# Performance work log

Measured on AMD Instinct MI355X. Metric: run time of the kernel, lower is better.

## Reference

```python
import jax, jax.numpy as jnp
import numpy as np

FRAME_LEN = 128
FFT_LEN = 128            # smallest power of 2 >= frame_length (TF default)
NUM_SPEC_BINS = FFT_LEN // 2 + 1  # 65
NUM_MEL = 80
SAMPLE_RATE = 16000.0
LOWER_HZ, UPPER_HZ = 80.0, 7600.0


def _hz_to_mel(f):
    # TF's HTK-style mel: 1127 * ln(1 + f/700)
    return 1127.0 * np.log1p(np.asarray(f, dtype=np.float64) / 700.0)


def _linear_to_mel_weight_matrix():
    # Faithful port of tf.signal.linear_to_mel_weight_matrix
    linear_freqs = np.linspace(0.0, SAMPLE_RATE / 2.0, NUM_SPEC_BINS)
    spec_mel = _hz_to_mel(linear_freqs[1:])[:, None]            # [64, 1] (bin 0 zeroed)
    edges = np.linspace(_hz_to_mel(LOWER_HZ), _hz_to_mel(UPPER_HZ), NUM_MEL + 2)
    lower, center, upper = edges[None, :-2], edges[None, 1:-1], edges[None, 2:]
    lower_slopes = (spec_mel - lower) / (center - lower)
    upper_slopes = (upper - spec_mel) / (upper - center)
    w = np.maximum(0.0, np.minimum(lower_slopes, upper_slopes))  # [64, 80]
    return np.pad(w, [[1, 0], [0, 0]]).astype(np.float32)        # [65, 80]


_MEL_W = jnp.asarray(_linear_to_mel_weight_matrix())


def setup_inputs() -> dict:
    key = jax.random.key(0)
    x = jax.random.normal(key, (16, 16384), dtype=jnp.float32)
    return {"x": x}


def reference(x):
    B, N = x.shape
    # pad_end=True with frame_step=1 -> N frames, pad FRAME_LEN-1 zeros at the end
    xp = jnp.pad(x, ((0, 0), (0, FRAME_LEN - 1)))
    idx = jnp.arange(N)[:, None] + jnp.arange(FRAME_LEN)[None, :]  # [N, 128]
    frames = xp[:, idx]                                            # [B, N, 128]
    n = jnp.arange(FRAME_LEN, dtype=jnp.float32)
    window = 0.5 - 0.5 * jnp.cos(2.0 * jnp.pi * n / FRAME_LEN)     # periodic Hann
    stft = jnp.fft.rfft(frames * window, n=FFT_LEN, axis=-1)       # [B, N, 65] complex
    mag = jax.lax.stop_gradient(jnp.abs(stft).astype(jnp.float32))
    mel = mag @ _MEL_W                                             # [B, N, 80]
    return jnp.concatenate([x[..., None], mel], axis=-1)           # [B, N, 81]
```

## Files before the change

### kernel.cpp

```cpp
#include <hip/hip_runtime.h>
#include <hip/hip_fp16.h>
#include <math.h>

#define B_SZ 16
#define N_SZ 16384
#define T_FR 128
#define NBIN 65
#define NMEL 80
#define ST   83
#define KN   6


constexpr float QC[33] = {
  1.0f,            0.99879545620f, 0.99518472667f, 0.98917650996f,
  0.98078528040f,  0.97003125319f, 0.95694033573f, 0.94154406518f,
  0.92387953251f,  0.90398929312f, 0.88192126435f, 0.85772861000f,
  0.83146961230f,  0.80320753148f, 0.77301045336f, 0.74095112535f,
  0.70710678119f,  0.67155895485f, 0.63439328416f, 0.59569930449f,
  0.55557023302f,  0.51410274419f, 0.47139673683f, 0.42755509343f,
  0.38268343236f,  0.33688985339f, 0.29028467725f, 0.24298017990f,
  0.19509032202f,  0.14673047446f, 0.09801714033f, 0.04906767433f,
  0.0f
};

__host__ __device__ constexpr float cosi(int k) {
  k = ((k % 128) + 128) % 128;
  return (k <= 32) ? QC[k]
       : (k <= 64) ? -QC[64 - k]
       : (k <= 96) ? -QC[k - 64]
       : QC[128 - k];
}
__host__ __device__ constexpr float sini(int k) { return cosi(k - 32); }
__host__ __device__ constexpr float hannw(int n) { return 0.5f - 0.5f * cosi(n); }
__host__ __device__ constexpr int rev6(int m) {
  return ((m & 1) << 5) | ((m & 2) << 3) | ((m & 4) << 1) |
         ((m & 8) >> 1) | ((m & 16) >> 3) | ((m & 32) >> 5);
}

constexpr double cln(double x) {
  int k = 0;
  while (x > 1.5)  { x *= 0.5; ++k; }
  while (x < 0.75) { x *= 2.0; --k; }
  const double y = (x - 1.0) / (x + 1.0);
  const double y2 = y * y;
  double t = y, s = 0.0;
  for (int i = 0; i < 40; ++i) { s += t / (double)(2 * i + 1); t *= y2; }
  return 2.0 * s + (double)k * 0.69314718055994530942;
}
constexpr double melf(double f) { return 1127.0 * cln(1.0 + f / 700.0); }

struct MelTab {
  int   kbe[NMEL];
  float w[NMEL][KN];
  constexpr MelTab() : kbe{}, w{} {
    const double mlo = melf(80.0), mhi = melf(7600.0);
    const double dm  = (mhi - mlo) / 81.0;
    for (int j = 0; j < NMEL; ++j) {
      const double lower = mlo + dm * (double)j;
      const double upper = lower + 2.0 * dm;
      int kb = 64;
      for (int k = 1; k < NBIN; ++k) {
        const double m = melf(125.0 * (double)k);
        const double a = m - lower, b2 = upper - m;
        if ((a < b2 ? a : b2) > 0.0) { kb = k; break; }
      }
      if (kb > NBIN - KN) kb = NBIN - KN;
      kbe[j] = kb;
      for (int r = 0; r < KN; ++r) {
        const int k = kb + r;
        double ww = 0.0;
        if (k >= 1 && k < NBIN) {
          const double m = melf(125.0 * (double)k);
          const double a = (m - lower) / dm, b2 = (upper - m) / dm;
          ww = a < b2 ? a : b2;
          if (ww < 0.0) ww = 0.0;
        }
        w[j][r] = (float)ww;
      }
    }
  }
};
constexpr MelTab MT{};


template <int LEN>
__device__ __forceinline__ void fft_stage(float (&zr)[64], float (&zi)[64]) {
#pragma unroll
  for (int i = 0; i < 64; i += LEN) {
#pragma unroll
    for (int j = 0; j < LEN / 2; ++j) {
      const int   q  = 128 * j / LEN;
      const float wr = cosi(q);
      const float wi = -sini(q);
      const int   a = i + j, bb = i + j + LEN / 2;
      const float br = zr[bb], bi = zi[bb];
      const float tr = wr * br - wi * bi;
      const float ti = wr * bi + wi * br;
      zr[bb] = zr[a] - tr;
      zi[bb] = zi[a] - ti;
      zr[a] += tr;
      zi[a] += ti;
    }
  }
}

__global__ __launch_bounds__(T_FR) void melspec_kernel(const float* __restrict__ x,
                                                       float* __restrict__ out) {
  __shared__ float  xs[T_FR + 128];
  __shared__ __half stage[T_FR * ST];

  const int tid = threadIdx.x;
  const int t0  = blockIdx.x * T_FR;
  const int b   = blockIdx.y;
  const float* xrow = x + (size_t)b * N_SZ;

  for (int i = tid; i < T_FR + 128; i += T_FR) {
    const int g = t0 + i;
    xs[i] = (g < N_SZ) ? xrow[g] : 0.0f;
  }
  __syncthreads();

  float zr[64], zi[64];
  {
    const float* xf = xs + tid;
#pragma unroll
    for (int m = 0; m < 64; ++m) {
      const int rm = rev6(m);
      zr[m] = xf[2 * rm]     * hannw(2 * rm);
      zi[m] = xf[2 * rm + 1] * hannw(2 * rm + 1);
    }
  }
  fft_stage<2>(zr, zi);
  fft_stage<4>(zr, zi);
  fft_stage<8>(zr, zi);
  fft_stage<16>(zr, zi);
  fft_stage<32>(zr, zi);
  fft_stage<64>(zr, zi);

  float mag[NBIN];
#pragma unroll
  for (int k = 0; k < NBIN; ++k) {
    const int ka = k & 63, kc = (64 - k) & 63;
    const float Ar = zr[ka], Ai = zi[ka];
    const float Br = zr[kc], Bi = zi[kc];
    const float c = cosi(k), s = sini(k);
    const float Xr = (Ar + Br) + c * (Ai + Bi) - s * (Ar - Br);
    const float Xi = (Ai - Bi) - c * (Ar - Br) - s * (Ai + Bi);
    mag[k] = 0.5f * sqrtf(Xr * Xr + Xi * Xi);
  }

  {
    __half* srow = stage + tid * ST;
    srow[0] = __float2half(xs[tid]);
#pragma unroll
    for (int j = 0; j < NMEL; ++j) {
      const int kb = MT.kbe[j];
      float acc = MT.w[j][0] * mag[kb];
#pragma unroll
      for (int r = 1; r < KN; ++r)
        acc = fmaf(MT.w[j][r], mag[kb + r], acc);
      srow[1 + j] = __float2half(acc);
    }
  }

  __syncthreads();

  float* orow = out + ((size_t)b * N_SZ + t0) * 81;
  int t = (tid >= 81) ? 1 : 0;
  int c = (tid >= 81) ? tid - 81 : tid;
  for (int i = 0; i < 81; ++i) {
    orow[i * T_FR + tid] = __half2float(stage[t * ST + c]);
    t += 1;
    c += 47;
    if (c >= 81) { c -= 81; ++t; }
  }
}

extern "C" void kernel_launch(void* const* d_in, const int* in_sizes, int n_in,
                              void* d_out, int out_size, void* d_ws, size_t ws_size,
                              hipStream_t stream) {
  const float* x = (const float*)d_in[0];
  float* out = (float*)d_out;
  dim3 grid(N_SZ / T_FR, B_SZ);
  dim3 block(T_FR);
  hipLaunchKernelGGL(melspec_kernel, grid, block, 0, stream, x, out);
}
```

Measured before the change: 119.0 us.

## Split each frame's FFT across two threads and partition mel projection across halves

Doubles the block to 256 threads so each 128-point FFT frame is handled by a thread pair. Each thread runs a 32-point FFT and the final radix-2 stage is done with cross-lane shuffles. Magnitudes are staged in shared memory as half precision, then the two thread halves each compute 40 mel bins using compile-time sparse filter tables. The intent is to cut per-thread register pressure (the 64-element complex arrays) and raise occupancy and parallelism. The cost is extra shuffles, an extra shared-memory pass and sync, and more fp16 rounding.

```diff
diff --git a/kernel.cpp b/kernel.cpp
--- a/kernel.cpp
+++ b/kernel.cpp
@@ -5,10 +5,12 @@
 #define B_SZ 16
 #define N_SZ 16384
 #define T_FR 128
+#define BLK  256
 #define NBIN 65
 #define NMEL 80
-#define ST   83
-#define KN   6
+#define MST  66
+#define SST  82
+#define KN2  5
 
 
 constexpr float QC[33] = {
@@ -22,7 +24,6 @@
   0.19509032202f,  0.14673047446f, 0.09801714033f, 0.04906767433f,
   0.0f
 };
-
 __host__ __device__ constexpr float cosi(int k) {
   k = ((k % 128) + 128) % 128;
   return (k <= 32) ? QC[k]
@@ -49,44 +50,49 @@
 }
 constexpr double melf(double f) { return 1127.0 * cln(1.0 + f / 700.0); }
 
-struct MelTab {
-  int   kbe[NMEL];
-  float w[NMEL][KN];
-  constexpr MelTab() : kbe{}, w{} {
+struct MelTab2 {
+  int   kb[NMEL];
+  float w[NMEL][KN2];
+  bool  ok0, ok1, okw;
+  constexpr MelTab2() : kb{}, w{}, ok0(true), ok1(true), okw(true) {
     const double mlo = melf(80.0), mhi = melf(7600.0);
     const double dm  = (mhi - mlo) / 81.0;
     for (int j = 0; j < NMEL; ++j) {
       const double lower = mlo + dm * (double)j;
       const double upper = lower + 2.0 * dm;
-      int kb = 64;
+      int b0 = -1, b1 = -1;
       for (int k = 1; k < NBIN; ++k) {
         const double m = melf(125.0 * (double)k);
-        const double a = m - lower, b2 = upper - m;
-        if ((a < b2 ? a : b2) > 0.0) { kb = k; break; }
-      }
-      if (kb > NBIN - KN) kb = NBIN - KN;
-      kbe[j] = kb;
-      for (int r = 0; r < KN; ++r) {
-        const int k = kb + r;
+        if (m - lower > 0.0 && upper - m > 0.0) { if (b0 < 0) b0 = k; b1 = k; }
+      }
+      if (b0 < 0) { b0 = 1; b1 = 0; }
+      kb[j] = b0;
+      for (int r = 0; r < KN2; ++r) {
+        const int k = b0 + r;
         double ww = 0.0;
-        if (k >= 1 && k < NBIN) {
+        if (k <= b1) {
           const double m = melf(125.0 * (double)k);
-          const double a = (m - lower) / dm, b2 = (upper - m) / dm;
-          ww = a < b2 ? a : b2;
-          if (ww < 0.0) ww = 0.0;
+          const double a = (m - lower) / dm, c = (upper - m) / dm;
+          ww = a < c ? a : c; if (ww < 0.0) ww = 0.0;
         }
         w[j][r] = (float)ww;
       }
+      if (b1 - b0 + 1 > KN2) okw = false;
+      if (j < 40) { if (b1 > 15) ok0 = false; }
+      else        { if (b0 < 12 || b1 > 64) ok1 = false; }
     }
   }
 };
-constexpr MelTab MT{};
+constexpr MelTab2 MT{};
+static_assert(MT.okw, "mel filter support wider than KN2");
+static_assert(MT.ok0, "low-half filters exceed bin 15");
+static_assert(MT.ok1, "high-half filters outside bins 12..64");
 
 
 template <int LEN>
-__device__ __forceinline__ void fft_stage(float (&zr)[64], float (&zi)[64]) {
-#pragma unroll
-  for (int i = 0; i < 64; i += LEN) {
+__device__ __forceinline__ void fft_stage32(float (&zr)[32], float (&zi)[32]) {
+#pragma unroll
+  for (int i = 0; i < 32; i += LEN) {
 #pragma unroll
     for (int j = 0; j < LEN / 2; ++j) {
       const int   q  = 128 * j / LEN;
@@ -104,75 +110,173 @@
   }
 }
 
-__global__ __launch_bounds__(T_FR) void melspec_kernel(const float* __restrict__ x,
-                                                       float* __restrict__ out) {
-  __shared__ float  xs[T_FR + 128];
-  __shared__ __half stage[T_FR * ST];
-
-  const int tid = threadIdx.x;
-  const int t0  = blockIdx.x * T_FR;
-  const int b   = blockIdx.y;
+__global__ __launch_bounds__(BLK) void melspec_kernel(const float* __restrict__ x,
+                                                      float* __restrict__ out) {
+  __shared__ float  xs[BLK];
+  __shared__ __half mags[T_FR * MST];
+  __shared__ __half stage[T_FR * SST];
+
+  const int i  = threadIdx.x;
+  const int t0 = blockIdx.x * T_FR;
+  const int b  = blockIdx.y;
   const float* xrow = x + (size_t)b * N_SZ;
 
-  for (int i = tid; i < T_FR + 128; i += T_FR) {
+  {
     const int g = t0 + i;
     xs[i] = (g < N_SZ) ? xrow[g] : 0.0f;
   }
   __syncthreads();
 
-  float zr[64], zi[64];
-  {
-    const float* xf = xs + tid;
-#pragma unroll
-    for (int m = 0; m < 64; ++m) {
+  const int t = i >> 1, h = i & 1;
+  float zr[32], zi[32];
+  {
+    const float* xf = xs + t;
+#pragma unroll
+    for (int m = 0; m < 32; ++m) {
       const int rm = rev6(m);
-      zr[m] = xf[2 * rm]     * hannw(2 * rm);
-      zi[m] = xf[2 * rm + 1] * hannw(2 * rm + 1);
-    }
-  }
-  fft_stage<2>(zr, zi);
-  fft_stage<4>(zr, zi);
-  fft_stage<8>(zr, zi);
-  fft_stage<16>(zr, zi);
-  fft_stage<32>(zr, zi);
-  fft_stage<64>(zr, zi);
-
-  float mag[NBIN];
-#pragma unroll
-  for (int k = 0; k < NBIN; ++k) {
-    const int ka = k & 63, kc = (64 - k) & 63;
-    const float Ar = zr[ka], Ai = zi[ka];
-    const float Br = zr[kc], Bi = zi[kc];
-    const float c = cosi(k), s = sini(k);
-    const float Xr = (Ar + Br) + c * (Ai + Bi) - s * (Ar - Br);
-    const float Xi = (Ai - Bi) - c * (Ar - Br) - s * (Ai + Bi);
-    mag[k] = 0.5f * sqrtf(Xr * Xr + Xi * Xi);
-  }
-
-  {
-    __half* srow = stage + tid * ST;
-    srow[0] = __float2half(xs[tid]);
-#pragma unroll
-    for (int j = 0; j < NMEL; ++j) {
-      const int kb = MT.kbe[j];
-      float acc = MT.w[j][0] * mag[kb];
-#pragma unroll
-      for (int r = 1; r < KN; ++r)
-        acc = fmaf(MT.w[j][r], mag[kb + r], acc);
-      srow[1 + j] = __float2half(acc);
-    }
-  }
-
+      const int n0 = 2 * rm + 2 * h;
+      const float w0 = h ? hannw(2 * rm + 2) : hannw(2 * rm);
+      const float w1 = h ? hannw(2 * rm + 3) : hannw(2 * rm + 1);
+      zr[m] = xf[n0]     * w0;
+      zi[m] = xf[n0 + 1] * w1;
+    }
+  }
+  fft_stage32<2>(zr, zi);
+  fft_stage32<4>(zr, zi);
+  fft_stage32<8>(zr, zi);
+  fft_stage32<16>(zr, zi);
+  fft_stage32<32>(zr, zi);
+
+  {
+    const float sgn = h ? -1.0f : 1.0f;
+#pragma unroll
+    for (int j = 0; j < 32; ++j) {
+      const float or_ = __shfl_xor(zr[j], 1, 64);
+      const float oi_ = __shfl_xor(zi[j], 1, 64);
+      const float zbr = h ? zr[j] : or_;
+      const float zbi = h ? zi[j] : oi_;
+      const float zar = h ? or_ : zr[j];
+      const float zai = h ? oi_ : zi[j];
+      const float wr = cosi(2 * j), wi = -sini(2 * j);
+      const float tr = wr * zbr - wi * zbi;
+      const float ti = wr * zbi + wi * zbr;
+      zr[j] = fmaf(sgn, tr, zar);
+      zi[j] = fmaf(sgn, ti, zai);
+    }
+  }
+
+  float mg[32];
+  float m64 = 0.0f;
+  {
+    const float er0 = __shfl_xor(zr[0], 1, 64);
+    const float ei0 = __shfl_xor(zi[0], 1, 64);
+    const float mag0  = fabsf(zr[0] + zi[0]);
+    const float mag32 = sqrtf(zr[0] * zr[0] + zi[0] * zi[0]);
+    mg[0] = h ? mag32 : mag0;
+    m64   = fabsf(er0 - ei0);
+#pragma unroll
+    for (int j = 1; j < 32; ++j) {
+      const float er = __shfl_xor(zr[32 - j], 1, 64);
+      const float ei = __shfl_xor(zi[32 - j], 1, 64);
+      const float Ar = zr[j], Ai = zi[j];
+      const float Br = er,    Bi = ei;
+      const float c = h ? -sini(j) : cosi(j);
+      const float s = h ?  cosi(j) : sini(j);
+      const float t1 = Ar + Br, t2 = Ai + Bi, t3 = Ar - Br, t4 = Ai - Bi;
+      float Xr = fmaf(c, t2, t1); Xr = fmaf(-s, t3, Xr);
+      float Xi = fmaf(-c, t3, t4); Xi = fmaf(-s, t2, Xi);
+      mg[j] = 0.5f * sqrtf(Xr * Xr + Xi * Xi);
+    }
+  }
+  {
+    __half2* mrow = (__half2*)(mags + t * MST + 32 * h);
+#pragma unroll
+    for (int p = 0; p < 16; ++p)
+      mrow[p] = __floats2half2_rn(mg[2 * p], mg[2 * p + 1]);
+    if (h) mags[t * MST + 64] = __float2half(m64);
+  }
   __syncthreads();
 
-  float* orow = out + ((size_t)b * N_SZ + t0) * 81;
-  int t = (tid >= 81) ? 1 : 0;
-  int c = (tid >= 81) ? tid - 81 : tid;
-  for (int i = 0; i < 81; ++i) {
-    orow[i * T_FR + tid] = __half2float(stage[t * ST + c]);
-    t += 1;
-    c += 47;
-    if (c >= 81) { c -= 81; ++t; }
+  {
+    const int t2 = i & 127;
+    const int H  = i >> 7;
+    __half* srow = stage + t2 * SST;
+    if (H == 0) {
+      float m0[16];
+      const __half2* mp = (const __half2*)(mags + t2 * MST);
+#pragma unroll
+      for (int p = 0; p < 8; ++p) {
+        const float2 f = __half22float2(mp[p]);
+        m0[2 * p] = f.x; m0[2 * p + 1] = f.y;
+      }
+      __half2* sp = (__half2*)(srow);
+#pragma unroll
+      for (int q = 0; q < 20; ++q) {
+        float acc[2];
+#pragma unroll
+        for (int e = 0; e < 2; ++e) {
+          const int j = 2 * q + e;
+          float a = 0.0f;
+#pragma unroll
+          for (int r = 0; r < KN2; ++r) {
+            const float ww = MT.w[j][r];
+            if (ww != 0.0f) {
+              int idx = MT.kb[j] + r; if (idx > 15) idx = 15;
+              a = fmaf(ww, m0[idx], a);
+            }
+          }
+          acc[e] = a;
+        }
+        sp[q] = __floats2half2_rn(acc[0], acc[1]);
+      }
+      srow[80] = __float2half(xs[t2]);
+    } else {
+      float m1[54];
+      const __half2* mp = (const __half2*)(mags + t2 * MST + 12);
+#pragma unroll
+      for (int p = 0; p < 27; ++p) {
+        const float2 f = __half22float2(mp[p]);
+        m1[2 * p] = f.x; m1[2 * p + 1] = f.y;
+      }
+      __half2* sp = (__half2*)(srow + 40);
+#pragma unroll
+      for (int q = 0; q < 20; ++q) {
+        float acc[2];
+#pragma unroll
+        for (int e = 0; e < 2; ++e) {
+          const int j = 40 + 2 * q + e;
+          float a = 0.0f;
+#pragma unroll
+          for (int r = 0; r < KN2; ++r) {
+            const float ww = MT.w[j][r];
+            if (ww != 0.0f) {
+              int idx = MT.kb[j] + r - 12; if (idx > 52) idx = 52;
+              a = fmaf(ww, m1[idx], a);
+            }
+          }
+          acc[e] = a;
+        }
+        sp[q] = __floats2half2_rn(acc[0], acc[1]);
+      }
+    }
+  }
+  __syncthreads();
+
+  {
+    float* orow = out + ((size_t)b * N_SZ + t0) * 81;
+    int tt = (i >= 243) ? 3 : (i >= 162) ? 2 : (i >= 81) ? 1 : 0;
+    int cc = i - 81 * tt;
+    int flat = i;
+#pragma unroll 1
+    for (int it = 0; it < 41; ++it) {
+      if (flat < T_FR * 81) {
+        const int m = (cc == 0) ? 80 : cc - 1;
+        orow[flat] = __half2float(stage[tt * SST + m]);
+      }
+      flat += BLK;
+      cc += 13; tt += 3;
+      if (cc >= 81) { cc -= 81; ++tt; }
+    }
   }
 }
 
@@ -182,6 +286,6 @@
   const float* x = (const float*)d_in[0];
   float* out = (float*)d_out;
   dim3 grid(N_SZ / T_FR, B_SZ);
-  dim3 block(T_FR);
+  dim3 block(BLK);
   hipLaunchKernelGGL(melspec_kernel, grid, block, 0, stream, x, out);
 }
```

Result: slower. 130.6 us (+9.8%).
